# Kernel optimization log

Measured on AMD Instinct MI355X. Metric: run time of the kernel, lower is better.

The kernel has to match this reference:

```python
import jax, jax.numpy as jnp
import numpy as np

DIM = 768
HEADS = 12
HEAD_DIM = DIM // HEADS
MLP_DIM = 4 * DIM
EPS = 1e-5


def setup_inputs() -> dict:
    key = jax.random.key(0)
    ks = jax.random.split(key, 8)
    s = lambda fan_in: 1.0 / np.sqrt(fan_in)
    return {
        "x": jax.random.normal(ks[0], (2, 2048, DIM), dtype=jnp.float32),
        "ln1_w": jnp.ones((DIM,), jnp.float32),
        "ln1_b": jnp.zeros((DIM,), jnp.float32),
        # weights stored [in, out]
        "qkv_w": jax.random.normal(ks[1], (DIM, 3 * DIM), jnp.float32) * s(DIM),
        "qkv_b": jnp.zeros((3 * DIM,), jnp.float32),
        "proj_w": jax.random.normal(ks[2], (DIM, DIM), jnp.float32) * s(DIM),
        "proj_b": jnp.zeros((DIM,), jnp.float32),
        "ln2_w": jnp.ones((DIM,), jnp.float32),
        "ln2_b": jnp.zeros((DIM,), jnp.float32),
        "lin1_w": jax.random.normal(ks[3], (DIM, MLP_DIM), jnp.float32) * s(DIM),
        "lin1_b": jnp.zeros((MLP_DIM,), jnp.float32),
        "lin2_w": jax.random.normal(ks[4], (MLP_DIM, DIM), jnp.float32) * s(MLP_DIM),
        "lin2_b": jnp.zeros((DIM,), jnp.float32),
    }


def _layernorm(x, w, b):
    mu = jnp.mean(x, axis=-1, keepdims=True)
    var = jnp.mean(jnp.square(x - mu), axis=-1, keepdims=True)
    return (x - mu) * jax.lax.rsqrt(var + EPS) * w + b


def _attention(x, qkv_w, qkv_b, proj_w, proj_b):
    B, N, C = x.shape
    qkv = (x @ qkv_w + qkv_b).reshape(B, N, 3, HEADS, HEAD_DIM)
    q, k, v = qkv[:, :, 0], qkv[:, :, 1], qkv[:, :, 2]  # [B, N, H, Dh]
    scale = HEAD_DIM ** -0.5
    attn = jnp.einsum("bqhd,bkhd->bhqk", q, k) * scale  # full NxN scores
    attn = jax.nn.softmax(attn, axis=-1)
    out = jnp.einsum("bhqk,bkhd->bqhd", attn, v).reshape(B, N, C)
    return out @ proj_w + proj_b


def reference(x, ln1_w, ln1_b, qkv_w, qkv_b, proj_w, proj_b,
              ln2_w, ln2_b, lin1_w, lin1_b, lin2_w, lin2_b):
    x = x + _attention(_layernorm(x, ln1_w, ln1_b), qkv_w, qkv_b, proj_w, proj_b)
    h = _layernorm(x, ln2_w, ln2_b)
    h = jax.nn.gelu(h @ lin1_w + lin1_b, approximate=False) @ lin2_w + lin2_b
    return x + h
```

## Files before the change

kernel.cpp:

```cpp
#include <hip/hip_runtime.h>
#include <hip/hip_bf16.h>
#include <math.h>

#define DIM 768
#define NTOK 4096
#define SEQ 2048
#define HEADS 12
#define HD 64

using bf16x8 = __attribute__((ext_vector_type(8))) __bf16;
using bf16x4 = __attribute__((ext_vector_type(4))) __bf16;
using short4v = __attribute__((ext_vector_type(4))) short;
using f32x4  = __attribute__((ext_vector_type(4))) float;
typedef unsigned short u16;

#define KEXPF 0.18033688011112042f

__device__ inline u16 f2bf(float f) {
  union { float f; unsigned u; } v; v.f = f;
  unsigned r = v.u + 0x7fffu + ((v.u >> 16) & 1u);
  return (u16)(r >> 16);
}

__device__ inline void pk2bf(float a, float b, u16* o0, u16* o1) {
  union { __hip_bfloat162 h; u16 u[2]; } cv;
  cv.h = __float22bfloat162_rn(make_float2(a, b));
  *o0 = cv.u[0];
  *o1 = cv.u[1];
}

__device__ inline unsigned pku32(float a, float b) {
  union { __hip_bfloat162 h; unsigned u; } cv;
  cv.h = __float22bfloat162_rn(make_float2(a, b));
  return cv.u;
}

__device__ inline float gelu_t(float x) {
  float z = x * (1.5957691216f + 0.0713548162f * x * x);
  return x / (1.0f + __expf(-z));
}

__device__ inline void gl_lds16(const u16* g, u16* l) {
  __builtin_amdgcn_global_load_lds(
      (const __attribute__((address_space(1))) unsigned int*)g,
      (__attribute__((address_space(3))) unsigned int*)l, 16, 0, 0);
}

__global__ __launch_bounds__(256) void ln_kernel(const float* __restrict__ x,
                                                 const float* __restrict__ w,
                                                 const float* __restrict__ b,
                                                 u16* __restrict__ y) {
  int row = blockIdx.x;
  int t = threadIdx.x;
  const float* xr = x + (size_t)row * DIM;
  float v0 = xr[t], v1 = xr[t + 256], v2 = xr[t + 512];
  float s = v0 + v1 + v2;
  float q = v0 * v0 + v1 * v1 + v2 * v2;
  for (int o = 32; o > 0; o >>= 1) {
    s += __shfl_down(s, o, 64);
    q += __shfl_down(q, o, 64);
  }
  __shared__ float ws_[4], wq_[4], mb[2];
  int wid = t >> 6;
  if ((t & 63) == 0) { ws_[wid] = s; wq_[wid] = q; }
  __syncthreads();
  if (t == 0) {
    float S = ws_[0] + ws_[1] + ws_[2] + ws_[3];
    float Q = wq_[0] + wq_[1] + wq_[2] + wq_[3];
    float mean = S * (1.0f / DIM);
    float var = Q * (1.0f / DIM) - mean * mean;
    mb[0] = mean;
    mb[1] = rsqrtf(var + 1e-5f);
  }
  __syncthreads();
  float mean = mb[0], rstd = mb[1];
  u16* yr = y + (size_t)row * DIM;
  yr[t]       = f2bf((v0 - mean) * rstd * w[t]       + b[t]);
  yr[t + 256] = f2bf((v1 - mean) * rstd * w[t + 256] + b[t + 256]);
  yr[t + 512] = f2bf((v2 - mean) * rstd * w[t + 512] + b[t + 512]);
}

__global__ __launch_bounds__(256) void redln_kernel(
    const float* __restrict__ P0, const float* __restrict__ P1,
    const float* __restrict__ bias, const float* __restrict__ res,
    float* __restrict__ x2, const float* __restrict__ lnw,
    const float* __restrict__ lnb, u16* __restrict__ y) {
  int row = blockIdx.x;
  int t = threadIdx.x;
  size_t off = (size_t)row * DIM;
  float v[3];
#pragma unroll
  for (int k = 0; k < 3; ++k) {
    int c = t + k * 256;
    v[k] = P0[off + c] + P1[off + c] + bias[c] + res[off + c];
    x2[off + c] = v[k];
  }
  float s = v[0] + v[1] + v[2];
  float q = v[0] * v[0] + v[1] * v[1] + v[2] * v[2];
  for (int o = 32; o > 0; o >>= 1) {
    s += __shfl_down(s, o, 64);
    q += __shfl_down(q, o, 64);
  }
  __shared__ float ws_[4], wq_[4], mb[2];
  int wid = t >> 6;
  if ((t & 63) == 0) { ws_[wid] = s; wq_[wid] = q; }
  __syncthreads();
  if (t == 0) {
    float S = ws_[0] + ws_[1] + ws_[2] + ws_[3];
    float Q = wq_[0] + wq_[1] + wq_[2] + wq_[3];
    float mean = S * (1.0f / DIM);
    float var = Q * (1.0f / DIM) - mean * mean;
    mb[0] = mean;
    mb[1] = rsqrtf(var + 1e-5f);
  }
  __syncthreads();
  float mean = mb[0], rstd = mb[1];
#pragma unroll
  for (int k = 0; k < 3; ++k) {
    int c = t + k * 256;
    y[off + c] = f2bf((v[k] - mean) * rstd * lnw[c] + lnb[c]);
  }
}

__global__ __launch_bounds__(256) void wcvt_all(
    const float* __restrict__ W0, const float* __restrict__ W1,
    const float* __restrict__ W2, const float* __restrict__ W3,
    u16* __restrict__ T0, u16* __restrict__ T1,
    u16* __restrict__ T2, u16* __restrict__ T3) {
  int id = blockIdx.x;
  const float* W; u16* Wt; int K, N, local;
  if (id < 1728)      { W = W0; Wt = T0; K = 768;  N = 2304; local = id; }
  else if (id < 2304) { W = W1; Wt = T1; K = 768;  N = 768;  local = id - 1728; }
  else if (id < 4608) { W = W2; Wt = T2; K = 768;  N = 3072; local = id - 2304; }
  else                { W = W3; Wt = T3; K = 3072; N = 768;  local = id - 4608; }
  int ntiles = N / 32;
  int n0 = (local % ntiles) * 32, k0 = (local / ntiles) * 32;
  __shared__ float tile[32][33];
  int tid = threadIdx.x;
  int c = tid & 31, r8 = tid >> 5;
#pragma unroll
  for (int p = 0; p < 4; ++p) {
    int k = r8 + p * 8;
    tile[k][c] = W[(size_t)(k0 + k) * N + n0 + c];
  }
  __syncthreads();
#pragma unroll
  for (int p = 0; p < 4; ++p) {
    int n = r8 + p * 8;
    Wt[(size_t)(n0 + n) * K + k0 + c] = f2bf(tile[c][n]);
  }
}

__global__ __launch_bounds__(256) void vtr_kernel(const u16* __restrict__ qkvB,
                                                  u16* __restrict__ vT) {
  __shared__ u16 tile[32][33];
  int v0 = blockIdx.x * 32, j0 = blockIdx.y * 32, b = blockIdx.z;
  int tid = threadIdx.x;
  int c = tid & 31, r8 = tid >> 5;
#pragma unroll
  for (int p = 0; p < 4; ++p) {
    int r = r8 + p * 8;
    tile[r][c] = qkvB[((size_t)(b * SEQ + j0 + r)) * 2304 + 1536 + v0 + c];
  }
  __syncthreads();
#pragma unroll
  for (int p = 0; p < 4; ++p) {
    int r = r8 + p * 8;
    vT[((size_t)(b * 768 + v0 + r)) * SEQ + j0 + c] = tile[c][r];
  }
}

__global__ __launch_bounds__(256) void bgemm_kernel(
    const u16* __restrict__ A, const u16* __restrict__ Bt,
    const float* __restrict__ bias, u16* __restrict__ Cb,
    int M, int N, int K, int act, int scaleq) {
  __shared__ __align__(16) u16 Asl[128 * 64];
  __shared__ __align__(16) u16 Bsl[128 * 64];
  int tid = threadIdx.x;
  int lane = tid & 63, wave = tid >> 6;
  int wm = wave >> 1, wn = wave & 1;
  int bm = blockIdx.y * 128, bn = blockIdx.x * 128;
  int l15 = lane & 15, quad = lane >> 4;
  int sm8 = tid >> 3;
  int kgx = (tid & 7) ^ (sm8 & 7);

  f32x4 acc[4][4] = {};
  const u16* Ap = A + (size_t)(bm + sm8) * K + kgx * 8;
  const u16* Bp = Bt + (size_t)(bn + sm8) * K + kgx * 8;
  u16* Al = &Asl[(wave * 8) * 64];
  u16* Bl = &Bsl[(wave * 8) * 64];
  int xr = l15 & 7;

  for (int k0 = 0; k0 < K; k0 += 64) {
#pragma unroll
    for (int p = 0; p < 4; ++p)
      gl_lds16(Ap + (size_t)(p * 32) * K + k0, Al + p * 32 * 64);
#pragma unroll
    for (int p = 0; p < 4; ++p)
      gl_lds16(Bp + (size_t)(p * 32) * K + k0, Bl + p * 32 * 64);
    __syncthreads();
#pragma unroll
    for (int ks = 0; ks < 2; ++ks) {
      int pu = ((ks << 2) + quad) ^ xr;
      bf16x8 af[4], bfr[4];
#pragma unroll
      for (int i = 0; i < 4; ++i) {
        af[i]  = *(const bf16x8*)&Asl[(wm * 64 + i * 16 + l15) * 64 + pu * 8];
        bfr[i] = *(const bf16x8*)&Bsl[(wn * 64 + i * 16 + l15) * 64 + pu * 8];
      }
#pragma unroll
      for (int i = 0; i < 4; ++i)
#pragma unroll
        for (int j = 0; j < 4; ++j)
          acc[i][j] = __builtin_amdgcn_mfma_f32_16x16x32_bf16(af[i], bfr[j], acc[i][j], 0, 0, 0);
    }
    __syncthreads();
  }

#pragma unroll
  for (int i = 0; i < 4; ++i) {
#pragma unroll
    for (int j = 0; j < 4; ++j) {
      int n = bn + wn * 64 + j * 16 + l15;
      float bv = bias[n];
      float cs = (scaleq && n < 768) ? KEXPF : 1.0f;
      float val[4];
#pragma unroll
      for (int r = 0; r < 4; ++r) {
        float v = (acc[i][j][r] + bv) * cs;
        val[r] = act ? gelu_t(v) : v;
      }
      u16 c0, c1, c2, c3;
      pk2bf(val[0], val[1], &c0, &c1);
      pk2bf(val[2], val[3], &c2, &c3);
      size_t mbase = (size_t)(bm + wm * 64 + i * 16 + quad * 4) * N + n;
      Cb[mbase]         = c0;
      Cb[mbase + N]     = c1;
      Cb[mbase + 2 * N] = c2;
      Cb[mbase + 3 * N] = c3;
    }
  }
}

__global__ __launch_bounds__(256) void bgemm_splitk(
    const u16* __restrict__ A, const u16* __restrict__ Bt,
    float* __restrict__ P0, float* __restrict__ P1,
    int M, int N, int K) {
  __shared__ __align__(16) u16 Asl[128 * 64];
  __shared__ __align__(16) u16 Bsl[64 * 64];
  int tid = threadIdx.x;
  int lane = tid & 63, wave = tid >> 6;
  int wm = wave >> 1, wn = wave & 1;
  int bm = blockIdx.y * 128, bn = blockIdx.x * 64;
  int l15 = lane & 15, quad = lane >> 4;
  int sm8 = tid >> 3;
  int kgx = (tid & 7) ^ (sm8 & 7);
  int half = K >> 1;
  int kbeg = blockIdx.z * half;

  f32x4 acc[4][2] = {};
  const u16* Ap = A + (size_t)(bm + sm8) * K + kbeg + kgx * 8;
  const u16* Bp = Bt + (size_t)(bn + sm8) * K + kbeg + kgx * 8;
  u16* Al = &Asl[(wave * 8) * 64];
  u16* Bl = &Bsl[(wave * 8) * 64];
  int xr = l15 & 7;

  for (int k0 = 0; k0 < half; k0 += 64) {
#pragma unroll
    for (int p = 0; p < 4; ++p)
      gl_lds16(Ap + (size_t)(p * 32) * K + k0, Al + p * 32 * 64);
#pragma unroll
    for (int p = 0; p < 2; ++p)
      gl_lds16(Bp + (size_t)(p * 32) * K + k0, Bl + p * 32 * 64);
    __syncthreads();
#pragma unroll
    for (int ks = 0; ks < 2; ++ks) {
      int pu = ((ks << 2) + quad) ^ xr;
      bf16x8 af[4], bfr[2];
#pragma unroll
      for (int i = 0; i < 4; ++i)
        af[i] = *(const bf16x8*)&Asl[(wm * 64 + i * 16 + l15) * 64 + pu * 8];
#pragma unroll
      for (int j = 0; j < 2; ++j)
        bfr[j] = *(const bf16x8*)&Bsl[(wn * 32 + j * 16 + l15) * 64 + pu * 8];
#pragma unroll
      for (int i = 0; i < 4; ++i)
#pragma unroll
        for (int j = 0; j < 2; ++j)
          acc[i][j] = __builtin_amdgcn_mfma_f32_16x16x32_bf16(af[i], bfr[j], acc[i][j], 0, 0, 0);
    }
    __syncthreads();
  }

  float* P = blockIdx.z ? P1 : P0;
#pragma unroll
  for (int i = 0; i < 4; ++i) {
#pragma unroll
    for (int j = 0; j < 2; ++j) {
      int n = bn + wn * 32 + j * 16 + l15;
#pragma unroll
      for (int r = 0; r < 4; ++r) {
        int m = bm + wm * 64 + i * 16 + quad * 4 + r;
        P[(size_t)m * N + n] = acc[i][j][r];
      }
    }
  }
}

__global__ __launch_bounds__(256) void red_kernel(
    const float* P0, const float* __restrict__ P1,
    const float* __restrict__ bias, const float* __restrict__ res,
    float* O, int Ncols) {
  int i = blockIdx.x * 256 + threadIdx.x;
  float4 a = ((const float4*)P0)[i];
  float4 b = ((const float4*)P1)[i];
  float4 r = ((const float4*)res)[i];
  int col = (i * 4) % Ncols;
  float4 bi = *(const float4*)&bias[col];
  float4 o;
  o.x = a.x + b.x + r.x + bi.x;
  o.y = a.y + b.y + r.y + bi.y;
  o.z = a.z + b.z + r.z + bi.z;
  o.w = a.w + b.w + r.w + bi.w;
  ((float4*)O)[i] = o;
}

#define LDP 68
__global__ __launch_bounds__(256, 3) void attn_kernel(const u16* __restrict__ qkv,
                                                      const u16* __restrict__ vT,
                                                      u16* __restrict__ out) {
  __shared__ __align__(16) char arena[40960];
  u16* Qsp = (u16*)arena;
  u16* Ksp = (u16*)(arena + 8192);
  u16* Vsp = (u16*)(arena + 24576);

  int tid = threadIdx.x;
  int lane = tid & 63, wave = tid >> 6;
  int l15 = lane & 15, quad = lane >> 4;
  int qt = blockIdx.x * 64;
  int h = blockIdx.y, b = blockIdx.z;
  size_t base = (size_t)b * SEQ;
  int srow = lane >> 3;
  int sux = (lane & 7) ^ (srow & 7);
  int r0 = wave * 16;
  const u16* qbase = qkv + (base + qt) * 2304 + h * HD;
  const u16* kbase = qkv + base * 2304 + 768 + h * HD;
  const u16* vbase = vT + ((size_t)(b * HEADS + h) * HD) * SEQ;

  gl_lds16(qbase + (size_t)(r0 + srow) * 2304 + sux * 8, Qsp + r0 * 64);
  gl_lds16(qbase + (size_t)(r0 + 8 + srow) * 2304 + sux * 8, Qsp + (r0 + 8) * 64);
  gl_lds16(kbase + (size_t)(r0 + srow) * 2304 + sux * 8, Ksp + r0 * 64);
  gl_lds16(kbase + (size_t)(r0 + 8 + srow) * 2304 + sux * 8, Ksp + (r0 + 8) * 64);
  gl_lds16(vbase + (size_t)(r0 + srow) * SEQ + sux * 8, Vsp + r0 * 64);
  gl_lds16(vbase + (size_t)(r0 + 8 + srow) * SEQ + sux * 8, Vsp + (r0 + 8) * 64);
  __syncthreads();

  int xr = l15 & 7;
  bf16x8 qf[4][2];
#pragma unroll
  for (int g = 0; g < 4; ++g)
#pragma unroll
    for (int s = 0; s < 2; ++s)
      qf[g][s] = *(const bf16x8*)&Qsp[(g * 16 + l15) * 64 + ((s * 4 + quad) ^ xr) * 8];

  gl_lds16(kbase + (size_t)(64 + r0 + srow) * 2304 + sux * 8, Ksp + 4096 + r0 * 64);
  gl_lds16(kbase + (size_t)(64 + r0 + 8 + srow) * 2304 + sux * 8, Ksp + 4096 + (r0 + 8) * 64);
  gl_lds16(vbase + (size_t)(r0 + srow) * SEQ + 64 + sux * 8, Vsp + 4096 + r0 * 64);
  gl_lds16(vbase + (size_t)(r0 + 8 + srow) * SEQ + 64 + sux * 8, Vsp + 4096 + (r0 + 8) * 64);

  int koff0 = (wave * 16 + l15) * 64 + ((quad ^ xr)) * 8;
  int koff1 = (wave * 16 + l15) * 64 + (((4 + quad) ^ xr)) * 8;
  int voff[4];
#pragma unroll
  for (int dg = 0; dg < 4; ++dg)
    voff[dg] = (dg * 16 + l15) * 64 + (((2 * wave + (quad >> 1)) ^ xr)) * 8 + (quad & 1) * 4;

  f32x4 oT[4][4] = {};
  f32x4 oT1[4] = {};
  const short4v ONES = {(short)0x3F80, (short)0x3F80, (short)0x3F80, (short)0x3F80};
  int buf = 0;

  for (int t = 0; t < 32; ++t) {
    const u16* Kb = Ksp + buf * 4096;
    const u16* Vb = Vsp + buf * 4096;

    f32x4 sT[4] = {};
    __builtin_amdgcn_s_setprio(1);
    {
      bf16x8 ak = *(const bf16x8*)&Kb[koff0];
#pragma unroll
      for (int g = 0; g < 4; ++g)
        sT[g] = __builtin_amdgcn_mfma_f32_16x16x32_bf16(ak, qf[g][0], sT[g], 0, 0, 0);
      bf16x8 ak1 = *(const bf16x8*)&Kb[koff1];
#pragma unroll
      for (int g = 0; g < 4; ++g)
        sT[g] = __builtin_amdgcn_mfma_f32_16x16x32_bf16(ak1, qf[g][1], sT[g], 0, 0, 0);
    }
    __builtin_amdgcn_s_setprio(0);

    short4v pb[4];
#pragma unroll
    for (int g = 0; g < 4; ++g) {
      float p0 = __builtin_amdgcn_exp2f(sT[g][0]);
      float p1 = __builtin_amdgcn_exp2f(sT[g][1]);
      float p2 = __builtin_amdgcn_exp2f(sT[g][2]);
      float p3 = __builtin_amdgcn_exp2f(sT[g][3]);
      union { unsigned u[2]; short4v s; } cv;
      cv.u[0] = pku32(p0, p1);
      cv.u[1] = pku32(p2, p3);
      pb[g] = cv.s;
    }

    short4v av[4];
#pragma unroll
    for (int dg = 0; dg < 4; ++dg)
      av[dg] = *(const short4v*)&Vb[voff[dg]];
    __builtin_amdgcn_s_setprio(1);
#pragma unroll
    for (int dg = 0; dg < 4; ++dg)
#pragma unroll
      for (int g = 0; g < 4; ++g)
        oT[dg][g] = __builtin_amdgcn_mfma_f32_16x16x16bf16_1k(av[dg], pb[g], oT[dg][g], 0, 0, 0);
#pragma unroll
    for (int g = 0; g < 4; ++g)
      oT1[g] = __builtin_amdgcn_mfma_f32_16x16x16bf16_1k(ONES, pb[g], oT1[g], 0, 0, 0);
    __builtin_amdgcn_s_setprio(0);

    __builtin_amdgcn_sched_barrier(0);
    __builtin_amdgcn_s_barrier();
    __builtin_amdgcn_sched_barrier(0);
    if (t < 30) {
      size_t kt2 = (size_t)(t + 2) * 64;
      u16* Kd = Ksp + buf * 4096;
      u16* Vd = Vsp + buf * 4096;
      gl_lds16(kbase + (kt2 + r0 + srow) * 2304 + sux * 8, Kd + r0 * 64);
      gl_lds16(kbase + (kt2 + r0 + 8 + srow) * 2304 + sux * 8, Kd + (r0 + 8) * 64);
      gl_lds16(vbase + (size_t)(r0 + srow) * SEQ + kt2 + sux * 8, Vd + r0 * 64);
      gl_lds16(vbase + (size_t)(r0 + 8 + srow) * SEQ + kt2 + sux * 8, Vd + (r0 + 8) * 64);
      asm volatile("s_waitcnt vmcnt(4)" ::: "memory");
    } else {
      asm volatile("s_waitcnt vmcnt(0)" ::: "memory");
    }
    __builtin_amdgcn_sched_barrier(0);
    __builtin_amdgcn_s_barrier();
    __builtin_amdgcn_sched_barrier(0);
    buf ^= 1;
  }

  float* LDSw = (float*)arena;
  float* lsd  = (float*)(arena + 17408);
  if (lane < 16) {
#pragma unroll
    for (int g = 0; g < 4; ++g) lsd[wave * 64 + g * 16 + lane] = oT1[g][0];
  }
  float linv = 0.f;
#pragma unroll
  for (int dg = 0; dg < 4; ++dg) {
#pragma unroll
    for (int g = 0; g < 4; ++g)
#pragma unroll
      for (int r = 0; r < 4; ++r)
        LDSw[wave * (16 * LDP) + (quad * 4 + r) * LDP + g * 16 + l15] = oT[dg][g][r];
    __syncthreads();
    if (dg == 0) {
      float L = lsd[wave * 16 + l15] + lsd[64 + wave * 16 + l15] +
                lsd[128 + wave * 16 + l15] + lsd[192 + wave * 16 + l15];
      linv = 1.0f / L;
    }
    float sv[4];
#pragma unroll
    for (int i = 0; i < 4; ++i) {
      int dloc = quad * 4 + i;
      float a = LDSw[dloc * LDP + wave * 16 + l15] +
                LDSw[1 * (16 * LDP) + dloc * LDP + wave * 16 + l15] +
                LDSw[2 * (16 * LDP) + dloc * LDP + wave * 16 + l15] +
                LDSw[3 * (16 * LDP) + dloc * LDP + wave * 16 + l15];
      sv[i] = a * linv;
    }
    size_t addr = (base + qt + wave * 16 + l15) * DIM + h * HD + dg * 16 + quad * 4;
    uint2 pk;
    pk.x = pku32(sv[0], sv[1]);
    pk.y = pku32(sv[2], sv[3]);
    *(uint2*)&out[addr] = pk;
    __syncthreads();
  }
}

extern "C" void kernel_launch(void* const* d_in, const int* in_sizes, int n_in,
                              void* d_out, int out_size, void* d_ws, size_t ws_size,
                              hipStream_t stream) {
  const float* x     = (const float*)d_in[0];
  const float* ln1w  = (const float*)d_in[1];
  const float* ln1b  = (const float*)d_in[2];
  const float* qkvw  = (const float*)d_in[3];
  const float* qkvbi = (const float*)d_in[4];
  const float* projw = (const float*)d_in[5];
  const float* projb = (const float*)d_in[6];
  const float* ln2w  = (const float*)d_in[7];
  const float* ln2b  = (const float*)d_in[8];
  const float* l1w   = (const float*)d_in[9];
  const float* l1b   = (const float*)d_in[10];
  const float* l2w   = (const float*)d_in[11];
  const float* l2b   = (const float*)d_in[12];
  float* out = (float*)d_out;

  char* w = (char*)d_ws;
  u16*   h     = (u16*)w;   w += (size_t)NTOK * DIM * 2;
  u16*   qkvB  = (u16*)w;
  u16*   mid   = (u16*)w;   w += (size_t)NTOK * 3072 * 2;
  u16*   attnb = (u16*)w;   w += (size_t)NTOK * DIM * 2;
  float* x2    = (float*)w; w += (size_t)NTOK * DIM * 4;
  u16*   vTb   = (u16*)w;   w += (size_t)NTOK * DIM * 2;
  u16*   qkvwt = (u16*)w;   w += (size_t)DIM * 2304 * 2;
  u16*   projwt= (u16*)w;   w += (size_t)DIM * DIM * 2;
  u16*   l1wt  = (u16*)w;   w += (size_t)DIM * 3072 * 2;
  u16*   l2wt  = (u16*)w;   w += (size_t)3072 * DIM * 2;
  float* Pbuf  = (float*)w; w += (size_t)NTOK * DIM * 4;

  wcvt_all<<<6912, 256, 0, stream>>>(qkvw, projw, l1w, l2w,
                                     qkvwt, projwt, l1wt, l2wt);

  ln_kernel<<<NTOK, 256, 0, stream>>>(x, ln1w, ln1b, h);
  bgemm_kernel<<<dim3(2304 / 128, NTOK / 128), 256, 0, stream>>>(
      h, qkvwt, qkvbi, qkvB, NTOK, 2304, DIM, 0, 1);
  vtr_kernel<<<dim3(768 / 32, SEQ / 32, 2), 256, 0, stream>>>(qkvB, vTb);
  attn_kernel<<<dim3(SEQ / 64, HEADS, 2), 256, 0, stream>>>(qkvB, vTb, attnb);

  bgemm_splitk<<<dim3(DIM / 64, NTOK / 128, 2), 256, 0, stream>>>(
      attnb, projwt, x2, Pbuf, NTOK, DIM, DIM);
  redln_kernel<<<NTOK, 256, 0, stream>>>(x2, Pbuf, projb, x, x2, ln2w, ln2b, h);

  bgemm_kernel<<<dim3(3072 / 128, NTOK / 128), 256, 0, stream>>>(
      h, l1wt, l1b, mid, NTOK, 3072, DIM, 1, 0);

  bgemm_splitk<<<dim3(DIM / 64, NTOK / 128, 2), 256, 0, stream>>>(
      mid, l2wt, out, Pbuf, NTOK, DIM, 3072);
  red_kernel<<<NTOK * DIM / 1024, 256, 0, stream>>>(out, Pbuf, l2b, x2, out, DIM);
}
```

Baseline: 279.6 us.

## Double-buffer GEMM LDS loads and remap workgroups across XCDs

Both GEMM kernels now keep two LDS buffers and prefetch the tile two steps ahead, using explicit vmcnt waits and raw barriers. Global loads then overlap with the MFMA work instead of stalling each iteration. All three kernels (GEMMs and attention) also remap the block index so consecutive tiles land on the same XCD, aiming for better L2 locality. The cost is doubled LDS use per block, which may lower occupancy, and the remap assumes the workgroup count divides evenly by 8.

```diff
diff --git a/kernel.cpp b/kernel.cpp
--- a/kernel.cpp
+++ b/kernel.cpp
@@ -174,12 +174,16 @@
     const u16* __restrict__ A, const u16* __restrict__ Bt,
     const float* __restrict__ bias, u16* __restrict__ Cb,
     int M, int N, int K, int act, int scaleq) {
-  __shared__ __align__(16) u16 Asl[128 * 64];
-  __shared__ __align__(16) u16 Bsl[128 * 64];
+  __shared__ __align__(16) u16 Asl[2][128 * 64];
+  __shared__ __align__(16) u16 Bsl[2][128 * 64];
+  int nwg = gridDim.x * gridDim.y;
+  int bid = blockIdx.y * gridDim.x + blockIdx.x;
+  int swz = (bid & 7) * (nwg >> 3) + (bid >> 3);
+  int bx = swz % gridDim.x, by = swz / gridDim.x;
   int tid = threadIdx.x;
   int lane = tid & 63, wave = tid >> 6;
   int wm = wave >> 1, wn = wave & 1;
-  int bm = blockIdx.y * 128, bn = blockIdx.x * 128;
+  int bm = by * 128, bn = bx * 128;
   int l15 = lane & 15, quad = lane >> 4;
   int sm8 = tid >> 3;
   int kgx = (tid & 7) ^ (sm8 & 7);
@@ -187,26 +191,33 @@
   f32x4 acc[4][4] = {};
   const u16* Ap = A + (size_t)(bm + sm8) * K + kgx * 8;
   const u16* Bp = Bt + (size_t)(bn + sm8) * K + kgx * 8;
-  u16* Al = &Asl[(wave * 8) * 64];
-  u16* Bl = &Bsl[(wave * 8) * 64];
   int xr = l15 & 7;
-
-  for (int k0 = 0; k0 < K; k0 += 64) {
+  int nk = K >> 6;
+
+  auto STAGE = [&](int k0, int sel) {
 #pragma unroll
     for (int p = 0; p < 4; ++p)
-      gl_lds16(Ap + (size_t)(p * 32) * K + k0, Al + p * 32 * 64);
+      gl_lds16(Ap + (size_t)(p * 32) * K + k0, &Asl[sel][(wave * 8 + p * 32) * 64]);
 #pragma unroll
     for (int p = 0; p < 4; ++p)
-      gl_lds16(Bp + (size_t)(p * 32) * K + k0, Bl + p * 32 * 64);
-    __syncthreads();
+      gl_lds16(Bp + (size_t)(p * 32) * K + k0, &Bsl[sel][(wave * 8 + p * 32) * 64]);
+  };
+
+  STAGE(0, 0);
+  if (nk > 1) STAGE(64, 1);
+  asm volatile("s_waitcnt vmcnt(8)" ::: "memory");
+  __builtin_amdgcn_s_barrier();
+
+  for (int t = 0; t < nk; ++t) {
+    int sel = t & 1;
 #pragma unroll
     for (int ks = 0; ks < 2; ++ks) {
       int pu = ((ks << 2) + quad) ^ xr;
       bf16x8 af[4], bfr[4];
 #pragma unroll
       for (int i = 0; i < 4; ++i) {
-        af[i]  = *(const bf16x8*)&Asl[(wm * 64 + i * 16 + l15) * 64 + pu * 8];
-        bfr[i] = *(const bf16x8*)&Bsl[(wn * 64 + i * 16 + l15) * 64 + pu * 8];
+        af[i]  = *(const bf16x8*)&Asl[sel][(wm * 64 + i * 16 + l15) * 64 + pu * 8];
+        bfr[i] = *(const bf16x8*)&Bsl[sel][(wn * 64 + i * 16 + l15) * 64 + pu * 8];
       }
 #pragma unroll
       for (int i = 0; i < 4; ++i)
@@ -214,7 +225,19 @@
         for (int j = 0; j < 4; ++j)
           acc[i][j] = __builtin_amdgcn_mfma_f32_16x16x32_bf16(af[i], bfr[j], acc[i][j], 0, 0, 0);
     }
-    __syncthreads();
+    if (t == nk - 1) break;
+    __builtin_amdgcn_sched_barrier(0);
+    __builtin_amdgcn_s_barrier();
+    __builtin_amdgcn_sched_barrier(0);
+    if (t + 2 < nk) {
+      STAGE((t + 2) << 6, sel);
+      asm volatile("s_waitcnt vmcnt(8)" ::: "memory");
+    } else {
+      asm volatile("s_waitcnt vmcnt(0)" ::: "memory");
+    }
+    __builtin_amdgcn_sched_barrier(0);
+    __builtin_amdgcn_s_barrier();
+    __builtin_amdgcn_sched_barrier(0);
   }
 
 #pragma unroll
@@ -246,12 +269,16 @@
     const u16* __restrict__ A, const u16* __restrict__ Bt,
     float* __restrict__ P0, float* __restrict__ P1,
     int M, int N, int K) {
-  __shared__ __align__(16) u16 Asl[128 * 64];
-  __shared__ __align__(16) u16 Bsl[64 * 64];
+  __shared__ __align__(16) u16 Asl[2][128 * 64];
+  __shared__ __align__(16) u16 Bsl[2][64 * 64];
+  int nwg = gridDim.x * gridDim.y;
+  int bid = blockIdx.y * gridDim.x + blockIdx.x;
+  int swz = (bid & 7) * (nwg >> 3) + (bid >> 3);
+  int bx = swz % gridDim.x, by = swz / gridDim.x;
   int tid = threadIdx.x;
   int lane = tid & 63, wave = tid >> 6;
   int wm = wave >> 1, wn = wave & 1;
-  int bm = blockIdx.y * 128, bn = blockIdx.x * 64;
+  int bm = by * 128, bn = bx * 64;
   int l15 = lane & 15, quad = lane >> 4;
   int sm8 = tid >> 3;
   int kgx = (tid & 7) ^ (sm8 & 7);
@@ -261,35 +288,54 @@
   f32x4 acc[4][2] = {};
   const u16* Ap = A + (size_t)(bm + sm8) * K + kbeg + kgx * 8;
   const u16* Bp = Bt + (size_t)(bn + sm8) * K + kbeg + kgx * 8;
-  u16* Al = &Asl[(wave * 8) * 64];
-  u16* Bl = &Bsl[(wave * 8) * 64];
   int xr = l15 & 7;
-
-  for (int k0 = 0; k0 < half; k0 += 64) {
+  int nk = half >> 6;
+
+  auto STAGE = [&](int k0, int sel) {
 #pragma unroll
     for (int p = 0; p < 4; ++p)
-      gl_lds16(Ap + (size_t)(p * 32) * K + k0, Al + p * 32 * 64);
+      gl_lds16(Ap + (size_t)(p * 32) * K + k0, &Asl[sel][(wave * 8 + p * 32) * 64]);
 #pragma unroll
     for (int p = 0; p < 2; ++p)
-      gl_lds16(Bp + (size_t)(p * 32) * K + k0, Bl + p * 32 * 64);
-    __syncthreads();
+      gl_lds16(Bp + (size_t)(p * 32) * K + k0, &Bsl[sel][(wave * 8 + p * 32) * 64]);
+  };
+
+  STAGE(0, 0);
+  if (nk > 1) STAGE(64, 1);
+  asm volatile("s_waitcnt vmcnt(6)" ::: "memory");
+  __builtin_amdgcn_s_barrier();
+
+  for (int t = 0; t < nk; ++t) {
+    int sel = t & 1;
 #pragma unroll
     for (int ks = 0; ks < 2; ++ks) {
       int pu = ((ks << 2) + quad) ^ xr;
       bf16x8 af[4], bfr[2];
 #pragma unroll
       for (int i = 0; i < 4; ++i)
-        af[i] = *(const bf16x8*)&Asl[(wm * 64 + i * 16 + l15) * 64 + pu * 8];
+        af[i] = *(const bf16x8*)&Asl[sel][(wm * 64 + i * 16 + l15) * 64 + pu * 8];
 #pragma unroll
       for (int j = 0; j < 2; ++j)
-        bfr[j] = *(const bf16x8*)&Bsl[(wn * 32 + j * 16 + l15) * 64 + pu * 8];
+        bfr[j] = *(const bf16x8*)&Bsl[sel][(wn * 32 + j * 16 + l15) * 64 + pu * 8];
 #pragma unroll
       for (int i = 0; i < 4; ++i)
 #pragma unroll
         for (int j = 0; j < 2; ++j)
           acc[i][j] = __builtin_amdgcn_mfma_f32_16x16x32_bf16(af[i], bfr[j], acc[i][j], 0, 0, 0);
     }
-    __syncthreads();
+    if (t == nk - 1) break;
+    __builtin_amdgcn_sched_barrier(0);
+    __builtin_amdgcn_s_barrier();
+    __builtin_amdgcn_sched_barrier(0);
+    if (t + 2 < nk) {
+      STAGE((t + 2) << 6, sel);
+      asm volatile("s_waitcnt vmcnt(6)" ::: "memory");
+    } else {
+      asm volatile("s_waitcnt vmcnt(0)" ::: "memory");
+    }
+    __builtin_amdgcn_sched_barrier(0);
+    __builtin_amdgcn_s_barrier();
+    __builtin_amdgcn_sched_barrier(0);
   }
 
   float* P = blockIdx.z ? P1 : P0;
@@ -334,11 +380,17 @@
   u16* Ksp = (u16*)(arena + 8192);
   u16* Vsp = (u16*)(arena + 24576);
 
+  int nwg = gridDim.x * gridDim.y * gridDim.z;
+  int bid = (blockIdx.z * gridDim.y + blockIdx.y) * gridDim.x + blockIdx.x;
+  int swz = (bid & 7) * (nwg >> 3) + (bid >> 3);
+  int bx = swz % gridDim.x;
+  int rem = swz / gridDim.x;
+  int h = rem % gridDim.y, b = rem / gridDim.y;
+
   int tid = threadIdx.x;
   int lane = tid & 63, wave = tid >> 6;
   int l15 = lane & 15, quad = lane >> 4;
-  int qt = blockIdx.x * 64;
-  int h = blockIdx.y, b = blockIdx.z;
+  int qt = bx * 64;
   size_t base = (size_t)b * SEQ;
   int srow = lane >> 3;
   int sux = (lane & 7) ^ (srow & 7);
```

Measured after the change: 277.7 us. Within noise of the previous version (-0.7%).
